# Performance work log

Measured on AMD Instinct MI355X. Metric: run time of the kernel, lower is better.

Reference implementation:

```python
import jax, jax.numpy as jnp
import numpy as np

_S = np.float32(1.0 / np.sqrt(2.0))
_lo = np.array([_S, _S], np.float32)   # dec_lo reversed == rec_lo for db1
_hi = np.array([_S, -_S], np.float32)  # dec_hi reversed == rec_hi for db1
# filters[k][i,j]: k=0 LL/2, k=1 hi(i)*lo(j), k=2 lo(i)*hi(j), k=3 hi*hi  (matches torch unsqueeze outer products)
DEC = np.stack([np.outer(_lo, _lo) / 2.0, np.outer(_hi, _lo), np.outer(_lo, _hi), np.outer(_hi, _hi)]).astype(np.float32)
INV = np.stack([np.outer(_lo, _lo) * 2.0, np.outer(_hi, _lo), np.outer(_lo, _hi), np.outer(_hi, _hi)]).astype(np.float32)
INV_FLIP = np.ascontiguousarray(INV[:, ::-1, ::-1])  # spatially flipped for conv_transpose-as-dilated-conv

DN = ('NCHW', 'OIHW', 'NCHW')


def wt(x):
    # single grouped (depthwise x4) strided conv == per-channel loop in the original
    N, C, H, W = x.shape
    k = jnp.broadcast_to(jnp.asarray(DEC)[None], (C, 4, 2, 2)).reshape(C * 4, 1, 2, 2)
    r = jax.lax.conv_general_dilated(x, k, (2, 2), 'VALID', dimension_numbers=DN, feature_group_count=C)
    r = r.reshape(N, C, 4, H // 2, W // 2)
    r = jnp.concatenate([r[:, :, :1], (r[:, :, 1:] + 1.0) / 2.0], axis=2)  # detail remap
    return r.reshape(N, 4 * C, H // 2, W // 2)


def iwt(v):
    N, C4, H, W = v.shape
    C = C4 // 4
    r = v.reshape(N, C, 4, H, W)
    r = jnp.concatenate([r[:, :, :1], 2.0 * r[:, :, 1:] - 1.0], axis=2).reshape(N, C4, H, W)
    k = jnp.broadcast_to(jnp.asarray(INV_FLIP)[None], (C, 4, 2, 2))
    # conv_transpose2d(stride=2, k=2) == dilated conv with lhs_dilation=2, pad 1, flipped kernel
    return jax.lax.conv_general_dilated(r, k, (1, 1), ((1, 1), (1, 1)), lhs_dilation=(2, 2),
                                        dimension_numbers=DN, feature_group_count=C)


def ws_conv(x, w, b, pad):
    # weight standardization: subtract mean over (in,kh,kw), divide by per-filter std (unbiased) + 1e-5
    wc = w - w.mean(axis=(1, 2, 3), keepdims=True)
    std = wc.reshape(w.shape[0], -1).std(axis=1, ddof=1).reshape(-1, 1, 1, 1) + 1e-5
    y = jax.lax.conv_general_dilated(x, wc / std, (1, 1), ((pad, pad), (pad, pad)), dimension_numbers=DN)
    return y if b is None else y + b[None, :, None, None]


def gn(x, g, b, G):
    N, C, H, W = x.shape
    xr = x.reshape(N, G, -1)
    m = xr.mean(-1, keepdims=True)
    v = xr.var(-1, keepdims=True)
    xr = (xr - m) * jax.lax.rsqrt(v + 1e-5)
    return xr.reshape(N, C, H, W) * g[None, :, None, None] + b[None, :, None, None]


def lrelu(t):
    return jnp.where(t > 0, t, 0.2 * t)


def setup_inputs() -> dict:
    key = jax.random.key(0)
    ks = iter(jax.random.split(key, 32))
    f32 = jnp.float32
    d = {}
    d['x'] = jax.random.normal(next(ks), (16, 3, 256, 256), f32)
    def wgt(shape):
        return 0.05 * jax.random.normal(next(ks), shape, f32)
    def bias(n):
        return 0.01 * jax.random.normal(next(ks), (n,), f32)
    c = 16
    d['conv1_w'], d['conv1_b'] = wgt((c, 12, 3, 3)), bias(c)
    d['conv2_w'], d['conv2_b'] = wgt((4 * c, 4 * c, 3, 3)), bias(4 * c)
    d['conv3_w'], d['conv3_b'] = wgt((16 * c, 16 * c, 3, 3)), bias(16 * c)
    d['conv4_w'], d['conv4_b'] = wgt((64 * c, 64 * c, 3, 3)), bias(64 * c)
    d['convd1_w'], d['convd1_b'] = wgt((12, c, 3, 3)), bias(12)
    d['convd2_w'], d['convd2_b'] = wgt((c, 2 * c, 3, 3)), bias(c)
    d['convd3_w'], d['convd3_b'] = wgt((4 * c, 8 * c, 3, 3)), bias(4 * c)
    d['convd4_w'], d['convd4_b'] = wgt((16 * c, 32 * c, 3, 3)), bias(16 * c)
    d['final_w'] = wgt((2, 3, 1, 1))
    for name, n in (('gn1', c), ('gn2', 4 * c), ('gn3', 16 * c), ('gn4', 64 * c)):
        d[name + '_w'] = 1.0 + 0.1 * jax.random.normal(next(ks), (n,), f32)
        d[name + '_b'] = 0.01 * jax.random.normal(next(ks), (n,), f32)
    return d


def reference(x, conv1_w, conv1_b, conv2_w, conv2_b, conv3_w, conv3_b, conv4_w, conv4_b,
              convd1_w, convd1_b, convd2_w, convd2_b, convd3_w, convd3_b, convd4_w, convd4_b,
              final_w, gn1_w, gn1_b, gn2_w, gn2_b, gn3_w, gn3_b, gn4_w, gn4_b):
    w1 = wt(x)
    c1 = gn(lrelu(ws_conv(w1, conv1_w, conv1_b, 1)), gn1_w, gn1_b, 2)
    w2 = wt(c1)
    c2 = gn(lrelu(ws_conv(w2, conv2_w, conv2_b, 1)), gn2_w, gn2_b, 8)
    w3 = wt(c2)
    c3 = gn(lrelu(ws_conv(w3, conv3_w, conv3_b, 1)), gn3_w, gn3_b, 32)
    w4 = wt(c3)
    c4 = gn(lrelu(ws_conv(w4, conv4_w, conv4_b, 1)), gn4_w, gn4_b, 128)
    c5 = gn(lrelu(ws_conv(c4, conv4_w, conv4_b, 1)), gn4_w, gn4_b, 128)
    c6 = ws_conv(c5, conv4_w, conv4_b, 1)
    ic4 = lrelu(c6 + w4)
    iw4 = jnp.concatenate([c3, iwt(ic4)], axis=1)
    ic3 = gn(lrelu(ws_conv(iw4, convd4_w, convd4_b, 1)), gn3_w, gn3_b, 32)
    iw3 = jnp.concatenate([c2, iwt(ic3)], axis=1)
    ic2 = gn(lrelu(ws_conv(iw3, convd3_w, convd3_b, 1)), gn2_w, gn2_b, 8)
    iw2 = jnp.concatenate([c1, iwt(ic2)], axis=1)
    ic1 = gn(lrelu(ws_conv(iw2, convd2_w, convd2_b, 1)), gn1_w, gn1_b, 2)
    iw1 = lrelu(ws_conv(ic1, convd1_w, convd1_b, 1))
    y = ws_conv(iwt(iw1), final_w, None, 0)
    return y
```

## Files before the change

### kernel.cpp

```cpp
#include <hip/hip_runtime.h>
#include <math.h>


#define NB 16

typedef _Float16 f16;
typedef _Float16 f16x8 __attribute__((ext_vector_type(8)));
typedef _Float16 f16x4 __attribute__((ext_vector_type(4)));
typedef float f32x4 __attribute__((ext_vector_type(4)));
typedef float f32x2 __attribute__((ext_vector_type(2)));
typedef unsigned int u32;

#define LLDS16(gp, lp)                                                          \
  __builtin_amdgcn_global_load_lds((const __attribute__((address_space(1))) u32*)(const void*)(gp), \
                                   (__attribute__((address_space(3))) u32*)(void*)(lp), 16, 0, 0)

__device__ __forceinline__ void ws_reduce(const float* wp, int fan, float* red,
                                          float& mean, float& inv) {
  float s = 0.f, s2 = 0.f;
  for (int i = threadIdx.x; i < fan; i += 256) { float v = wp[i]; s += v; s2 += v * v; }
  red[threadIdx.x] = s; red[256 + threadIdx.x] = s2;
  __syncthreads();
  for (int st = 128; st > 0; st >>= 1) {
    if (threadIdx.x < st) {
      red[threadIdx.x] += red[threadIdx.x + st];
      red[256 + threadIdx.x] += red[256 + threadIdx.x + st];
    }
    __syncthreads();
  }
  float sum = red[0], sumsq = red[256];
  mean = sum / (float)fan;
  float var = (sumsq - sum * mean) / (float)(fan - 1);
  if (var < 0.f) var = 0.f;
  inv = 1.0f / (sqrtf(var) + 1e-5f);
}

__global__ void ws_all_kernel(const float* w0, float* o0, const float* w1, float* o1,
                              const float* w2, float* o2, const float* w3, float* o3) {
  __shared__ float red[512];
  int b = blockIdx.x;
  const float* w; float* o; int fan, oi;
  if (b < 16)      { w = w0; o = o0; fan = 108; oi = b; }
  else if (b < 28) { w = w1; o = o1; fan = 144; oi = b - 16; }
  else if (b < 44) { w = w2; o = o2; fan = 288; oi = b - 28; }
  else             { w = w3; o = o3; fan = 3;   oi = b - 44; }
  const float* wp = w + (size_t)oi * fan;
  float mean, inv; ws_reduce(wp, fan, red, mean, inv);
  for (int i = threadIdx.x; i < fan; i += 256)
    o[(size_t)oi * fan + i] = (wp[i] - mean) * inv;
}

__global__ void ws_f16_all_kernel(const float* w0, f16* o0, const float* w1, f16* o1,
                                  const float* w2, f16* o2, const float* w3, f16* o3,
                                  const float* w4, f16* o4) {
  __shared__ float red[512];
  int b = blockIdx.x;
  const float* w; f16* o; int fan, Cin, Cout, oi;
  if (b < 64)        { w = w0; o = o0; fan = 576;  Cin = 64;   Cout = 64;   oi = b; }
  else if (b < 320)  { w = w1; o = o1; fan = 2304; Cin = 256;  Cout = 256;  oi = b - 64; }
  else if (b < 1344) { w = w2; o = o2; fan = 9216; Cin = 1024; Cout = 1024; oi = b - 320; }
  else if (b < 1408) { w = w3; o = o3; fan = 1152; Cin = 128;  Cout = 64;   oi = b - 1344; }
  else               { w = w4; o = o4; fan = 4608; Cin = 512;  Cout = 256;  oi = b - 1408; }
  const float* wp = w + (size_t)oi * fan;
  float mean, inv; ws_reduce(wp, fan, red, mean, inv);
  for (int i = threadIdx.x; i < fan; i += 256) {
    int ci = i / 9, tap = i - ci * 9;
    o[((size_t)tap * Cout + oi) * Cin + ci] = (f16)((wp[i] - mean) * inv);
  }
}

__device__ __forceinline__ void halo_write(f16* buf, int C, int H, int W, int t) {
  int c8s = C >> 3;
  int c8 = t % c8s; int q = t / c8s;
  int P = 2 * (W + 2) + 2 * H;
  int b = q % P; int n = q / P;
  int y, x;
  if (b < W + 2) { y = 0; x = b; }
  else if (b < 2 * (W + 2)) { y = H + 1; x = b - (W + 2); }
  else { int bb = b - 2 * (W + 2); y = 1 + (bb >> 1); x = (bb & 1) ? (W + 1) : 0; }
  size_t a = (((size_t)n * (H + 2) + y) * (W + 2) + x) * C + c8 * 8;
  *(f16x8*)(buf + a) = (f16x8){0, 0, 0, 0, 0, 0, 0, 0};
}

__global__ void halo2_kernel(f16* b0, int c0, int h0, int w0, int n0,
                             f16* b1, int c1, int h1, int w1, int total) {
  int idx = blockIdx.x * 256 + threadIdx.x;
  if (idx >= total) return;
  if (idx < n0) halo_write(b0, c0, h0, w0, idx);
  else halo_write(b1, c1, h1, w1, idx - n0);
}

__global__ void zero_halo_kernel(f16* __restrict__ buf, int C, int H, int W, int total8) {
  int idx = blockIdx.x * 256 + threadIdx.x;
  if (idx >= total8) return;
  halo_write(buf, C, H, W, idx);
}

__global__ void wt_kernel(const float* __restrict__ in, float* __restrict__ out,
                          int C, int Ho, int Wo, int total) {
  int idx = blockIdx.x * 256 + threadIdx.x;
  if (idx >= total) return;
  int w = idx % Wo; int t = idx / Wo;
  int h = t % Ho; t /= Ho;
  int c = t % C; int n = t / C;
  int Wi = 2 * Wo;
  const float* ip = in + (((size_t)n * C + c) * (2 * Ho) + 2 * h) * Wi + 2 * w;
  float a = ip[0], b = ip[1], cc = ip[Wi], d = ip[Wi + 1];
  size_t cs = (size_t)Ho * Wo;
  float* op = out + (((size_t)n * 4 * C + 4 * c) * Ho + h) * Wo + w;
  op[0]      = 0.25f * (a + b + cc + d);
  op[cs]     = 0.25f * (a + b - cc - d) + 0.5f;
  op[2 * cs] = 0.25f * (a - b + cc - d) + 0.5f;
  op[3 * cs] = 0.25f * (a - b - cc + d) + 0.5f;
}

__global__ __launch_bounds__(256) void wt_nhwc_gn_kernel(
    const float* __restrict__ in, const float* __restrict__ gnp,
    const float* __restrict__ gamma, const float* __restrict__ beta,
    int G, int Sg, int len,
    f16* __restrict__ out, float* __restrict__ out32, float* __restrict__ gnwb,
    int C, int Ho, int Wo) {
  __shared__ f16 sm[32][264];
  __shared__ float scs[8], shs[8];
  int HWo = Ho * Wo;
  int p0 = blockIdx.x * 256, c0 = blockIdx.y * 8, n = blockIdx.z;
  int t = threadIdx.x;
  if (t < 8) {
    int c = c0 + t;
    int g = c / (C / G);
    const float* pp = gnp + (size_t)((n * G + g) * Sg) * 2;
    float s = 0.f, s2 = 0.f;
    for (int i = 0; i < Sg; ++i) { s += pp[2 * i]; s2 += pp[2 * i + 1]; }
    float mean = s / (float)len;
    float var = s2 / (float)len - mean * mean;
    if (var < 0.f) var = 0.f;
    float inv = rsqrtf(var + 1e-5f);
    float ga = gamma[c];
    scs[t] = inv * ga;
    shs[t] = beta[c] - mean * inv * ga;
  }
  __syncthreads();
  int p = p0 + t; int h = p / Wo; int ww = p - h * Wo;
  int Wi = 2 * Wo;
  int C4 = 4 * C;
#pragma unroll
  for (int r = 0; r < 8; ++r) {
    size_t ioff = (((size_t)n * C + c0 + r) * (2 * Ho) + 2 * h) * Wi + 2 * ww;
    const float* ip = in + ioff;
    f32x2 u0 = *(const f32x2*)ip;
    f32x2 u1 = *(const f32x2*)(ip + Wi);
    float sc = scs[r], sh = shs[r];
    float a = u0.x * sc + sh, b = u0.y * sc + sh;
    float cc = u1.x * sc + sh, d = u1.y * sc + sh;
    if (gnwb) {
      float* wp = gnwb + ioff;
      *(f32x2*)wp = (f32x2){a, b};
      *(f32x2*)(wp + Wi) = (f32x2){cc, d};
    }
    float v0 = 0.25f * (a + b + cc + d);
    float v1 = 0.25f * (a + b - cc - d) + 0.5f;
    float v2 = 0.25f * (a - b + cc - d) + 0.5f;
    float v3 = 0.25f * (a - b - cc + d) + 0.5f;
    sm[4 * r][t]     = (f16)v0;
    sm[4 * r + 1][t] = (f16)v1;
    sm[4 * r + 2][t] = (f16)v2;
    sm[4 * r + 3][t] = (f16)v3;
    if (out32) {
      float* op = out32 + (((size_t)n * C4 + 4 * (c0 + r)) * Ho + h) * Wo + ww;
      size_t cs = (size_t)HWo;
      op[0] = v0; op[cs] = v1; op[2 * cs] = v2; op[3 * cs] = v3;
    }
  }
  __syncthreads();
#pragma unroll
  for (int i = 0; i < 4; ++i) {
    int c = t + i * 256;
    int pl = c >> 2, cio = (c & 3) * 8;
    f16x8 v;
#pragma unroll
    for (int u = 0; u < 8; ++u) v[u] = sm[cio + u][pl];
    int pp = p0 + pl; int y = pp / Wo; int x = pp - y * Wo;
    *(f16x8*)(out + (((size_t)n * (Ho + 2) + y + 1) * (Wo + 2) + x + 1) * C4 + c0 * 4 + cio) = v;
  }
}

__global__ void concat_iwt_kernel(const float* __restrict__ skip, const float* __restrict__ v,
                                  float* __restrict__ out, const float* __restrict__ gnp,
                                  const float* __restrict__ gamma, const float* __restrict__ beta,
                                  int G, int Sg, int len, int C, int Hh, int Wh,
                                  int totalA, int total) {
  int idx = blockIdx.x * 256 + threadIdx.x;
  if (idx >= total) return;
  int W = 2 * Wh, H = 2 * Hh; int HWs = H * W;
  if (idx < totalA) {
    int p = idx % HWs; int t = idx / HWs; int c = t % C; int n = t / C;
    out[((size_t)n * 2 * C + c) * HWs + p] = skip[idx];
    return;
  }
  int i2 = idx - totalA;
  int w = i2 % Wh; int t = i2 / Wh; int h = t % Hh; t /= Hh;
  int c = t % C; int n = t / C;
  size_t cs = (size_t)Hh * Wh;
  const float* vp = v + (((size_t)n * 4 * C + 4 * c) * Hh + h) * Wh + w;
  float v0 = vp[0], v1 = vp[cs], v2 = vp[2 * cs], v3 = vp[3 * cs];
  if (gnp) {
    int cpg = (4 * C) / G;
    int g = (4 * c) / cpg;
    const float* pp = gnp + (size_t)((n * G + g) * Sg) * 2;
    float s = 0.f, s2 = 0.f;
    for (int i = 0; i < Sg; ++i) { s += pp[2 * i]; s2 += pp[2 * i + 1]; }
    float mean = s / (float)len;
    float var = s2 / (float)len - mean * mean;
    if (var < 0.f) var = 0.f;
    float inv = rsqrtf(var + 1e-5f);
    v0 = (v0 - mean) * inv * gamma[4 * c]     + beta[4 * c];
    v1 = (v1 - mean) * inv * gamma[4 * c + 1] + beta[4 * c + 1];
    v2 = (v2 - mean) * inv * gamma[4 * c + 2] + beta[4 * c + 2];
    v3 = (v3 - mean) * inv * gamma[4 * c + 3] + beta[4 * c + 3];
  }
  v1 = 2.f * v1 - 1.f; v2 = 2.f * v2 - 1.f; v3 = 2.f * v3 - 1.f;
  float* op = out + (((size_t)n * 2 * C + C + c) * H + 2 * h) * (size_t)W + 2 * w;
  op[0]     = v0 + 0.5f * ( v1 + v2 + v3);
  op[1]     = v0 + 0.5f * ( v1 - v2 - v3);
  op[W]     = v0 + 0.5f * (-v1 + v2 - v3);
  op[W + 1] = v0 + 0.5f * (-v1 - v2 + v3);
}

__global__ __launch_bounds__(256) void to_nhwc_pad_kernel(const float* __restrict__ in,
                                                          f16* __restrict__ out,
                                                          int C, int H, int W) {
  __shared__ f16 sm[32][264];
  int HW = H * W;
  int p0 = blockIdx.x * 256, c0 = blockIdx.y * 32, n = blockIdx.z;
  int t = threadIdx.x;
  const float* ip = in + ((size_t)n * C + c0) * HW + p0;
#pragma unroll 8
  for (int r = 0; r < 32; ++r) sm[r][t] = (f16)ip[(size_t)r * HW + t];
  __syncthreads();
#pragma unroll
  for (int i = 0; i < 4; ++i) {
    int c = t + i * 256;
    int pl = c >> 2, cio = (c & 3) * 8;
    f16x8 v;
#pragma unroll
    for (int u = 0; u < 8; ++u) v[u] = sm[cio + u][pl];
    int p = p0 + pl; int y = p / W; int x = p - y * W;
    *(f16x8*)(out + (((size_t)n * (H + 2) + y + 1) * (W + 2) + x + 1) * C + c0 + cio) = v;
  }
}

__global__ __launch_bounds__(256) void gn_nhwc_kernel(
    const float* __restrict__ in, const float* __restrict__ gnp,
    const float* __restrict__ gamma, const float* __restrict__ beta,
    f16* __restrict__ out, int C, int H, int W, int G, int Sg, int len) {
  __shared__ f16 sm[32][264];
  int HW = H * W;
  int p0 = blockIdx.x * 256, c0 = blockIdx.y * 32, n = blockIdx.z;
  int t = threadIdx.x;
  int cpg = C / G;
  const float* ip = in + ((size_t)n * C + c0) * HW + p0;
#pragma unroll 8
  for (int r = 0; r < 32; ++r) {
    int c = c0 + r; int g = c / cpg;
    const float* pp = gnp + (size_t)((n * G + g) * Sg) * 2;
    float s = 0.f, s2 = 0.f;
    for (int i = 0; i < Sg; ++i) { s += pp[2 * i]; s2 += pp[2 * i + 1]; }
    float mean = s / (float)len;
    float var = s2 / (float)len - mean * mean;
    if (var < 0.f) var = 0.f;
    float inv = rsqrtf(var + 1e-5f);
    float ga = gamma[c], be = beta[c];
    sm[r][t] = (f16)((ip[(size_t)r * HW + t] - mean) * inv * ga + be);
  }
  __syncthreads();
#pragma unroll
  for (int i = 0; i < 4; ++i) {
    int c = t + i * 256;
    int pl = c >> 2, cio = (c & 3) * 8;
    f16x8 v;
#pragma unroll
    for (int u = 0; u < 8; ++u) v[u] = sm[cio + u][pl];
    int p = p0 + pl; int y = p / W; int x = p - y * W;
    *(f16x8*)(out + (((size_t)n * (H + 2) + y + 1) * (W + 2) + x + 1) * C + c0 + cio) = v;
  }
}

__global__ __launch_bounds__(256) void conv_mfma6_kernel(
    const f16* __restrict__ A, const f16* __restrict__ Wp,
    f16* __restrict__ part, int Cin, int H, int W, int Cout, int HW) {
  constexpr int CH = 128 * 64;
  __shared__ f16 Asm[2 * CH];
  __shared__ f16 Bsm[2 * CH];

  const int tid = threadIdx.x;
  const int w = tid >> 6, lane = tid & 63;
  const int m0 = blockIdx.x * 128;
  const int co0 = blockIdx.y * 128;
  const int Wp2 = W + 2;

  const f16* gA[4]; const f16* gB[4];
  int lOff[4];
#pragma unroll
  for (int e = 0; e < 4; ++e) {
    int c = e * 256 + tid;
    int r = c >> 3, j = c & 7;
    int jx = j ^ (r & 7);
    int m = m0 + r; int n = m / HW; int p = m - n * HW;
    int y = p / W; int x = p - y * W;
    gA[e] = A + (((size_t)n * (H + 2) + y + 1) * Wp2 + (x + 1)) * Cin + jx * 8;
    gB[e] = Wp + (size_t)(co0 + r) * Cin + jx * 8;
    lOff[e] = (e * 256 + w * 64) * 8;
  }

  const int wm = w & 1, wn = w >> 1;
  const int lr = lane & 15, quad = lane >> 4;
  int aoffs[4][2], boffs[4][2];
#pragma unroll
  for (int i = 0; i < 4; ++i)
#pragma unroll
    for (int kk = 0; kk < 2; ++kk) {
      int r = wm * 64 + i * 16 + lr;
      int cidx = kk * 4 + quad;
      aoffs[i][kk] = (r * 8 + (cidx ^ (r & 7))) * 8;
      int rb = wn * 64 + i * 16 + lr;
      boffs[i][kk] = (rb * 8 + (cidx ^ (rb & 7))) * 8;
    }

  f32x4 acc[4][4];
#pragma unroll
  for (int i = 0; i < 4; ++i)
#pragma unroll
    for (int j = 0; j < 4; ++j) acc[i][j] = (f32x4){0.f, 0.f, 0.f, 0.f};

  const int kpt = Cin >> 6;
  const int nit = (9 * kpt) / gridDim.z;
  const int it0 = blockIdx.z * nit;
  const size_t bstride = (size_t)Cout * Cin;

  auto stageAB = [&](int it, int sel) {
    int tap = it / kpt, kk = it - tap * kpt;
    int dy = tap / 3 - 1, dx = tap % 3 - 1;
    long offA = ((long)dy * Wp2 + dx) * Cin + (kk << 6);
    long offB = (long)tap * bstride + (kk << 6);
    f16* ab = Asm + sel * CH;
    f16* bb = Bsm + sel * CH;
#pragma unroll
    for (int e = 0; e < 4; ++e) {
      LLDS16(gA[e] + offA, ab + lOff[e]);
      LLDS16(gB[e] + offB, bb + lOff[e]);
    }
  };

  stageAB(it0, 0);
  int sel = 0;
  for (int ii = 0; ii < nit; ++ii) {
    __syncthreads();
    if (ii + 1 < nit) stageAB(it0 + ii + 1, sel ^ 1);
    const f16* ab = Asm + sel * CH;
    const f16* bb = Bsm + sel * CH;
    f16x8 af[4][2], bf[4][2];
#pragma unroll
    for (int i = 0; i < 4; ++i)
#pragma unroll
      for (int kk = 0; kk < 2; ++kk) {
        af[i][kk] = *(const f16x8*)&ab[aoffs[i][kk]];
        bf[i][kk] = *(const f16x8*)&bb[boffs[i][kk]];
      }
#pragma unroll
    for (int kk = 0; kk < 2; ++kk)
#pragma unroll
      for (int i = 0; i < 4; ++i)
#pragma unroll
        for (int j = 0; j < 4; ++j)
          acc[i][j] = __builtin_amdgcn_mfma_f32_16x16x32_f16(af[i][kk], bf[j][kk], acc[i][j], 0, 0, 0);
    sel ^= 1;
  }

  const size_t pbase = (size_t)blockIdx.z * NB * Cout * HW;
#pragma unroll
  for (int i = 0; i < 4; ++i) {
    int mg = m0 + wm * 64 + i * 16 + quad * 4;
    int n = mg / HW, p = mg - n * HW;
#pragma unroll
    for (int j = 0; j < 4; ++j) {
      int co = co0 + wn * 64 + j * 16 + lr;
      f32x4 v = acc[i][j];
      f16x4 h;
#pragma unroll
      for (int r = 0; r < 4; ++r) h[r] = (f16)v[r];
      *(f16x4*)&part[pbase + ((size_t)n * Cout + co) * HW + p] = h;
    }
  }
}

__global__ __launch_bounds__(256) void reduceS_kernel(
    const f16* __restrict__ part, const float* __restrict__ bias,
    const float* __restrict__ add, float* __restrict__ out,
    int Cout, int HW, int S, int do_lrelu, int total4,
    float* __restrict__ gnp, int G, int Sg) {
  __shared__ float red[512];
  int idx = blockIdx.x * 256 + threadIdx.x;
  if (idx >= total4) return;
  size_t sstride = (size_t)NB * Cout * HW;
  int hw4 = HW >> 2;
  int p4 = idx % hw4; int t = idx / hw4;
  int c = t % Cout;
  size_t eoff = (size_t)t * HW + p4 * 4;
  float b = bias[c];
  f32x4 o = {b, b, b, b};
  for (int s = 0; s < S; ++s) {
    f16x4 a = *(const f16x4*)(part + s * sstride + eoff);
#pragma unroll
    for (int r = 0; r < 4; ++r) o[r] += (float)a[r];
  }
  if (add) {
    f32x4 av = *(const f32x4*)(add + eoff);
#pragma unroll
    for (int r = 0; r < 4; ++r) o[r] += av[r];
  }
  if (do_lrelu)
#pragma unroll
    for (int r = 0; r < 4; ++r) o[r] = o[r] > 0.f ? o[r] : 0.2f * o[r];
  *(f32x4*)(out + eoff) = o;
  if (gnp) {
    float ls = o[0] + o[1] + o[2] + o[3];
    float ls2 = o[0]*o[0] + o[1]*o[1] + o[2]*o[2] + o[3]*o[3];
    red[threadIdx.x] = ls; red[256 + threadIdx.x] = ls2;
    __syncthreads();
    for (int st = 128; st > 0; st >>= 1) {
      if (threadIdx.x < st) {
        red[threadIdx.x] += red[threadIdx.x + st];
        red[256 + threadIdx.x] += red[256 + threadIdx.x + st];
      }
      __syncthreads();
    }
    if (threadIdx.x == 0) {
      int flat0 = blockIdx.x * 1024;
      int chw = Cout * HW;
      int n = flat0 / chw;
      int rem = flat0 - n * chw;
      int L = (Cout / G) * HW;
      int g = rem / L;
      int s = (rem - g * L) >> 10;
      gnp[((n * G + g) * Sg + s) * 2] = red[0];
      gnp[((n * G + g) * Sg + s) * 2 + 1] = red[256];
    }
  }
}

__global__ __launch_bounds__(256) void conv_mfma3_kernel(
    const f16* __restrict__ A, const f16* __restrict__ Wp,
    const float* __restrict__ bias, float* __restrict__ out,
    int Cin, int H, int W, int Cout, int HW, int do_lrelu) {
  constexpr int CHA = 128 * 64;
  constexpr int CHB = 64 * 64;
  __shared__ f16 Asm[2 * CHA];
  __shared__ f16 Bsm[2 * CHB];

  const int tid = threadIdx.x;
  const int w = tid >> 6, lane = tid & 63;
  const int m0 = blockIdx.x * 128;
  const int co0 = blockIdx.y * 64;
  const int Wp2 = W + 2;

  const f16* gA[4];
  int lAoff[4];
#pragma unroll
  for (int e = 0; e < 4; ++e) {
    int c = e * 256 + tid;
    int r = c >> 3, j = c & 7;
    int jx = j ^ (r & 7);
    int m = m0 + r; int n = m / HW; int p = m - n * HW;
    int y = p / W; int x = p - y * W;
    gA[e] = A + (((size_t)n * (H + 2) + y + 1) * Wp2 + (x + 1)) * Cin + jx * 8;
    lAoff[e] = (e * 256 + w * 64) * 8;
  }
  const f16* gB[2];
  int lBoff[2];
#pragma unroll
  for (int e = 0; e < 2; ++e) {
    int c = e * 256 + tid;
    int r = c >> 3, j = c & 7;
    int jx = j ^ (r & 7);
    gB[e] = Wp + (size_t)(co0 + r) * Cin + jx * 8;
    lBoff[e] = (e * 256 + w * 64) * 8;
  }

  const int wm = w & 1, wn = w >> 1;
  const int lr = lane & 15, quad = lane >> 4;
  int aoffs[4][2], boffs[2][2];
#pragma unroll
  for (int i = 0; i < 4; ++i)
#pragma unroll
    for (int kk = 0; kk < 2; ++kk) {
      int r = wm * 64 + i * 16 + lr;
      int cidx = kk * 4 + quad;
      aoffs[i][kk] = (r * 8 + (cidx ^ (r & 7))) * 8;
    }
#pragma unroll
  for (int jn = 0; jn < 2; ++jn)
#pragma unroll
    for (int kk = 0; kk < 2; ++kk) {
      int rb = wn * 32 + jn * 16 + lr;
      int cidx = kk * 4 + quad;
      boffs[jn][kk] = (rb * 8 + (cidx ^ (rb & 7))) * 8;
    }

  f32x4 acc[4][2];
#pragma unroll
  for (int i = 0; i < 4; ++i)
#pragma unroll
    for (int jn = 0; jn < 2; ++jn) acc[i][jn] = (f32x4){0.f, 0.f, 0.f, 0.f};

  const int kpt = Cin >> 6;
  const int nit = 9 * kpt;
  const size_t bstride = (size_t)Cout * Cin;

  auto stageAB = [&](int it, int sel) {
    int tap = it / kpt, kk = it - tap * kpt;
    int dy = tap / 3 - 1, dx = tap % 3 - 1;
    long offA = ((long)dy * Wp2 + dx) * Cin + (kk << 6);
    long offB = (long)tap * bstride + (kk << 6);
    f16* ab = Asm + sel * CHA;
    f16* bb = Bsm + sel * CHB;
#pragma unroll
    for (int e = 0; e < 4; ++e) LLDS16(gA[e] + offA, ab + lAoff[e]);
#pragma unroll
    for (int e = 0; e < 2; ++e) LLDS16(gB[e] + offB, bb + lBoff[e]);
  };

  stageAB(0, 0);
  int sel = 0;
  for (int ii = 0; ii < nit; ++ii) {
    __syncthreads();
    if (ii + 1 < nit) stageAB(ii + 1, sel ^ 1);
    const f16* ab = Asm + sel * CHA;
    const f16* bb = Bsm + sel * CHB;
    f16x8 af[4][2], bf[2][2];
#pragma unroll
    for (int i = 0; i < 4; ++i)
#pragma unroll
      for (int kk = 0; kk < 2; ++kk) af[i][kk] = *(const f16x8*)&ab[aoffs[i][kk]];
#pragma unroll
    for (int jn = 0; jn < 2; ++jn)
#pragma unroll
      for (int kk = 0; kk < 2; ++kk) bf[jn][kk] = *(const f16x8*)&bb[boffs[jn][kk]];
#pragma unroll
    for (int kk = 0; kk < 2; ++kk)
#pragma unroll
      for (int i = 0; i < 4; ++i)
#pragma unroll
        for (int jn = 0; jn < 2; ++jn)
          acc[i][jn] = __builtin_amdgcn_mfma_f32_16x16x32_f16(af[i][kk], bf[jn][kk], acc[i][jn], 0, 0, 0);
    sel ^= 1;
  }

#pragma unroll
  for (int i = 0; i < 4; ++i) {
    int mg = m0 + wm * 64 + i * 16 + quad * 4;
    int n = mg / HW, p = mg - n * HW;
#pragma unroll
    for (int jn = 0; jn < 2; ++jn) {
      int co = co0 + wn * 32 + jn * 16 + lr;
      float b = bias[co];
      f32x4 v = acc[i][jn];
#pragma unroll
      for (int r = 0; r < 4; ++r) {
        float u = v[r] + b;
        v[r] = (do_lrelu && u < 0.f) ? 0.2f * u : u;
      }
      *(f32x4*)&out[((size_t)n * Cout + co) * HW + p] = v;
    }
  }
}

template <int CO, int CIC>
__global__ __launch_bounds__(256) void conv3x3_kernel(
    const float* __restrict__ in, const float* __restrict__ wgt,
    const float* __restrict__ bias, float* __restrict__ out,
    int Cin, int H, int W, int Cout, int do_lrelu, float* __restrict__ gnp) {
  __shared__ float sm[CIC][18][18];
  int tiles_x = W >> 4;
  int bt = blockIdx.x;
  int tx0 = (bt % tiles_x) << 4;
  int ty0 = (bt / tiles_x) << 4;
  int co0 = blockIdx.y * CO;
  int n = blockIdx.z;
  int tid = threadIdx.x;
  int lx = tid & 15, ly = tid >> 4;

  float acc[CO];
#pragma unroll
  for (int i = 0; i < CO; i++) acc[i] = 0.f;

  const float* inb = in + (size_t)n * Cin * H * W;

  for (int ci0 = 0; ci0 < Cin; ci0 += CIC) {
    __syncthreads();
    for (int idx = tid; idx < CIC * 324; idx += 256) {
      int ci = idx / 324;
      int r = idx - ci * 324;
      int gy = r / 18, gx = r - gy * 18;
      int iy = ty0 + gy - 1, ix = tx0 + gx - 1;
      float v = 0.f;
      if ((unsigned)iy < (unsigned)H && (unsigned)ix < (unsigned)W)
        v = inb[((size_t)(ci0 + ci)) * H * W + (size_t)iy * W + ix];
      sm[ci][gy][gx] = v;
    }
    __syncthreads();
#pragma unroll
    for (int ci = 0; ci < CIC; ci++) {
      float x00 = sm[ci][ly][lx],     x01 = sm[ci][ly][lx + 1],     x02 = sm[ci][ly][lx + 2];
      float x10 = sm[ci][ly + 1][lx], x11 = sm[ci][ly + 1][lx + 1], x12 = sm[ci][ly + 1][lx + 2];
      float x20 = sm[ci][ly + 2][lx], x21 = sm[ci][ly + 2][lx + 1], x22 = sm[ci][ly + 2][lx + 2];
      const float* wp = wgt + ((size_t)co0 * Cin + (ci0 + ci)) * 9;
#pragma unroll
      for (int co = 0; co < CO; co++) {
        const float* wc = wp + (size_t)co * Cin * 9;
        float a = acc[co];
        a = fmaf(wc[0], x00, a); a = fmaf(wc[1], x01, a); a = fmaf(wc[2], x02, a);
        a = fmaf(wc[3], x10, a); a = fmaf(wc[4], x11, a); a = fmaf(wc[5], x12, a);
        a = fmaf(wc[6], x20, a); a = fmaf(wc[7], x21, a); a = fmaf(wc[8], x22, a);
        acc[co] = a;
      }
    }
  }

  float vout[CO];
#pragma unroll
  for (int co = 0; co < CO; co++) {
    float v = acc[co] + bias[co0 + co];
    if (do_lrelu) v = v > 0.f ? v : 0.2f * v;
    vout[co] = v;
  }

  if (gnp) {
    float p0 = 0.f, q0 = 0.f, p1 = 0.f, q1 = 0.f;
#pragma unroll
    for (int co = 0; co < 8; ++co) { p0 += vout[co]; q0 += vout[co] * vout[co]; }
#pragma unroll
    for (int co = 8; co < CO; ++co) { p1 += vout[co]; q1 += vout[co] * vout[co]; }
    float* red = &sm[0][0][0];
    __syncthreads();
    red[tid] = p0; red[256 + tid] = q0; red[512 + tid] = p1; red[768 + tid] = q1;
    __syncthreads();
    for (int st = 128; st > 0; st >>= 1) {
      if (tid < st) {
        red[tid] += red[tid + st]; red[256 + tid] += red[256 + tid + st];
        red[512 + tid] += red[512 + tid + st]; red[768 + tid] += red[768 + tid + st];
      }
      __syncthreads();
    }
    if (tid == 0) {
      int S = gridDim.x;
      gnp[((n * 2 + 0) * S + blockIdx.x) * 2]     = red[0];
      gnp[((n * 2 + 0) * S + blockIdx.x) * 2 + 1] = red[256];
      gnp[((n * 2 + 1) * S + blockIdx.x) * 2]     = red[512];
      gnp[((n * 2 + 1) * S + blockIdx.x) * 2 + 1] = red[768];
    }
  }

  int oy = ty0 + ly, ox = tx0 + lx;
#pragma unroll
  for (int co = 0; co < CO; co++)
    out[(((size_t)n * Cout + co0 + co) * H + oy) * W + ox] = vout[co];
}

template <int CO, int CIC>
__global__ __launch_bounds__(256) void conv3x3_iwt_kernel(
    const float* __restrict__ in, const float* __restrict__ wgt,
    const float* __restrict__ bias, const float* __restrict__ fw,
    const float* __restrict__ gnp, const float* __restrict__ gamma,
    const float* __restrict__ beta, int G, int Sg, int len,
    float* __restrict__ out, int Cin, int H, int W) {
  __shared__ float sm[CIC][18][18];
  __shared__ float csc[16], csh[16];
  int tiles_x = W >> 4;
  int bt = blockIdx.x;
  int tx0 = (bt % tiles_x) << 4;
  int ty0 = (bt / tiles_x) << 4;
  int n = blockIdx.z;
  int tid = threadIdx.x;
  int lx = tid & 15, ly = tid >> 4;

  if (tid < Cin) {
    int g = tid / (Cin / G);
    const float* pp = gnp + (size_t)((n * G + g) * Sg) * 2;
    float s = 0.f, s2 = 0.f;
    for (int i = 0; i < Sg; ++i) { s += pp[2 * i]; s2 += pp[2 * i + 1]; }
    float mean = s / (float)len;
    float var = s2 / (float)len - mean * mean;
    if (var < 0.f) var = 0.f;
    float inv = rsqrtf(var + 1e-5f);
    float ga = gamma[tid];
    csc[tid] = inv * ga;
    csh[tid] = beta[tid] - mean * inv * ga;
  }
  __syncthreads();

  float acc[CO];
#pragma unroll
  for (int i = 0; i < CO; i++) acc[i] = 0.f;

  const float* inb = in + (size_t)n * Cin * H * W;

  for (int ci0 = 0; ci0 < Cin; ci0 += CIC) {
    __syncthreads();
    for (int idx = tid; idx < CIC * 324; idx += 256) {
      int ci = idx / 324;
      int r = idx - ci * 324;
      int gy = r / 18, gx = r - gy * 18;
      int iy = ty0 + gy - 1, ix = tx0 + gx - 1;
      float v = 0.f;
      if ((unsigned)iy < (unsigned)H && (unsigned)ix < (unsigned)W)
        v = inb[((size_t)(ci0 + ci)) * H * W + (size_t)iy * W + ix] * csc[ci0 + ci] + csh[ci0 + ci];
      sm[ci][gy][gx] = v;
    }
    __syncthreads();
#pragma unroll
    for (int ci = 0; ci < CIC; ci++) {
      float x00 = sm[ci][ly][lx],     x01 = sm[ci][ly][lx + 1],     x02 = sm[ci][ly][lx + 2];
      float x10 = sm[ci][ly + 1][lx], x11 = sm[ci][ly + 1][lx + 1], x12 = sm[ci][ly + 1][lx + 2];
      float x20 = sm[ci][ly + 2][lx], x21 = sm[ci][ly + 2][lx + 1], x22 = sm[ci][ly + 2][lx + 2];
      const float* wp = wgt + (size_t)(ci0 + ci) * 9;
#pragma unroll
      for (int co = 0; co < CO; co++) {
        const float* wc = wp + (size_t)co * Cin * 9;
        float a = acc[co];
        a = fmaf(wc[0], x00, a); a = fmaf(wc[1], x01, a); a = fmaf(wc[2], x02, a);
        a = fmaf(wc[3], x10, a); a = fmaf(wc[4], x11, a); a = fmaf(wc[5], x12, a);
        a = fmaf(wc[6], x20, a); a = fmaf(wc[7], x21, a); a = fmaf(wc[8], x22, a);
        acc[co] = a;
      }
    }
  }

  float vout[CO];
#pragma unroll
  for (int co = 0; co < CO; co++) {
    float v = acc[co] + bias[co];
    vout[co] = v > 0.f ? v : 0.2f * v;
  }

  float y0[3], y1[3], y2[3], y3[3];
#pragma unroll
  for (int c = 0; c < 3; ++c) {
    float v0 = vout[4 * c];
    float v1 = 2.f * vout[4 * c + 1] - 1.f;
    float v2 = 2.f * vout[4 * c + 2] - 1.f;
    float v3 = 2.f * vout[4 * c + 3] - 1.f;
    y0[c] = v0 + 0.5f * ( v1 + v2 + v3);
    y1[c] = v0 + 0.5f * ( v1 - v2 - v3);
    y2[c] = v0 + 0.5f * (-v1 + v2 - v3);
    y3[c] = v0 + 0.5f * (-v1 - v2 + v3);
  }
  float w0 = fw[0], w1 = fw[1], w2 = fw[2], w3 = fw[3], w4 = fw[4], w5 = fw[5];
  int oy = ty0 + ly, ox = tx0 + lx;
  int OW = 2 * W;
  size_t ocs = (size_t)(2 * H) * OW;
  float* o0 = out + (size_t)n * 2 * ocs + (size_t)(2 * oy) * OW + 2 * ox;
  o0[0]      = w0 * y0[0] + w1 * y0[1] + w2 * y0[2];
  o0[1]      = w0 * y1[0] + w1 * y1[1] + w2 * y1[2];
  o0[OW]     = w0 * y2[0] + w1 * y2[1] + w2 * y2[2];
  o0[OW + 1] = w0 * y3[0] + w1 * y3[1] + w2 * y3[2];
  float* o1 = o0 + ocs;
  o1[0]      = w3 * y0[0] + w4 * y0[1] + w5 * y0[2];
  o1[1]      = w3 * y1[0] + w4 * y1[1] + w5 * y1[2];
  o1[OW]     = w3 * y2[0] + w4 * y2[1] + w5 * y2[2];
  o1[OW + 1] = w3 * y3[0] + w4 * y3[1] + w5 * y3[2];
}

__global__ __launch_bounds__(256) void gn_stats_kernel(const float* __restrict__ x,
                                                       float* __restrict__ part,
                                                       int C, int HW, int G, int SPLIT) {
  __shared__ float red[512];
  int gs = blockIdx.x;
  int g = gs / SPLIT, s = gs - g * SPLIT;
  int n = blockIdx.y;
  int cpg = C / G;
  int len = cpg * HW;
  int chunk = len / SPLIT;
  size_t base = ((size_t)n * C + (size_t)g * cpg) * HW + (size_t)s * chunk;
  const f32x4* xp = (const f32x4*)(x + base);
  int chunk4 = chunk >> 2;
  float sm = 0.f, s2 = 0.f;
  for (int i = threadIdx.x; i < chunk4; i += 256) {
    f32x4 v = xp[i];
    sm += v.x + v.y + v.z + v.w;
    s2 += v.x * v.x + v.y * v.y + v.z * v.z + v.w * v.w;
  }
  red[threadIdx.x] = sm; red[256 + threadIdx.x] = s2;
  __syncthreads();
  for (int st = 128; st > 0; st >>= 1) {
    if (threadIdx.x < st) {
      red[threadIdx.x] += red[threadIdx.x + st];
      red[256 + threadIdx.x] += red[256 + threadIdx.x + st];
    }
    __syncthreads();
  }
  if (threadIdx.x == 0) {
    int o = ((n * G + g) * SPLIT + s) * 2;
    part[o] = red[0]; part[o + 1] = red[256];
  }
}


extern "C" void kernel_launch(void* const* d_in, const int* in_sizes, int n_in,
                              void* d_out, int out_size, void* d_ws, size_t ws_size,
                              hipStream_t stream) {
  const float* x        = (const float*)d_in[0];
  const float* conv1_w  = (const float*)d_in[1];
  const float* conv1_b  = (const float*)d_in[2];
  const float* conv2_w  = (const float*)d_in[3];
  const float* conv2_b  = (const float*)d_in[4];
  const float* conv3_w  = (const float*)d_in[5];
  const float* conv3_b  = (const float*)d_in[6];
  const float* conv4_w  = (const float*)d_in[7];
  const float* conv4_b  = (const float*)d_in[8];
  const float* convd1_w = (const float*)d_in[9];
  const float* convd1_b = (const float*)d_in[10];
  const float* convd2_w = (const float*)d_in[11];
  const float* convd2_b = (const float*)d_in[12];
  const float* convd3_w = (const float*)d_in[13];
  const float* convd3_b = (const float*)d_in[14];
  const float* convd4_w = (const float*)d_in[15];
  const float* convd4_b = (const float*)d_in[16];
  const float* final_w  = (const float*)d_in[17];
  const float* gn1_w = (const float*)d_in[18];
  const float* gn1_b = (const float*)d_in[19];
  const float* gn2_w = (const float*)d_in[20];
  const float* gn2_b = (const float*)d_in[21];
  const float* gn3_w = (const float*)d_in[22];
  const float* gn3_b = (const float*)d_in[23];
  const float* gn4_w = (const float*)d_in[24];
  const float* gn4_b = (const float*)d_in[25];

  char* base = (char*)d_ws;
  size_t off = 0;
  auto allocB = [&](size_t bytes) { size_t o = off; off = (off + bytes + 255) & ~(size_t)255; return o; };

  size_t o_sw1  = allocB(16 * 108 * 4);
  size_t o_swd1 = allocB(12 * 144 * 4);
  size_t o_swd2 = allocB(16 * 288 * 4);
  size_t o_swf  = allocB(6 * 4);
  size_t o_pw2  = allocB((size_t)9 * 64 * 64 * 2);
  size_t o_pw3  = allocB((size_t)9 * 256 * 256 * 2);
  size_t o_pw4  = allocB((size_t)9 * 1024 * 1024 * 2);
  size_t o_pwd3 = allocB((size_t)9 * 64 * 128 * 2);
  size_t o_pwd4 = allocB((size_t)9 * 256 * 512 * 2);
  size_t o_R1   = allocB((size_t)NB * 66 * 66 * 128 * 2);
  size_t o_R2   = allocB((size_t)NB * 34 * 34 * 512 * 2);
  size_t o_gnp  = allocB(16384 * 4);
  size_t o_c1 = allocB((size_t)NB * 16 * 128 * 128 * 4);
  size_t o_c2 = allocB((size_t)NB * 64 * 64 * 64 * 4);
  size_t o_c3 = allocB((size_t)NB * 256 * 32 * 32 * 4);
  size_t o_w4 = allocB((size_t)NB * 1024 * 16 * 16 * 4);
  size_t o_t1 = allocB((size_t)NB * 1024 * 16 * 16 * 4);
  size_t o_t2 = allocB((size_t)NB * 512 * 32 * 32 * 4);

  if (off > ws_size) return;

  float* c1 = (float*)(base + o_c1);
  float* c2 = (float*)(base + o_c2);
  float* c3 = (float*)(base + o_c3);
  float* w4 = (float*)(base + o_w4);
  float* t1 = (float*)(base + o_t1);
  float* t2 = (float*)(base + o_t2);
  f16* part  = (f16*)(base + o_R1);
  f16* ah64  = (f16*)(base + o_R1);
  f16* ah128 = (f16*)(base + o_R1);
  f16* ah256 = (f16*)(base + o_R2);
  f16* ah1k  = (f16*)(base + o_R2);
  f16* ah512 = (f16*)(base + o_R2);
  f16* pw2 = (f16*)(base + o_pw2);
  f16* pw3 = (f16*)(base + o_pw3);
  f16* pw4 = (f16*)(base + o_pw4);
  f16* pwd3 = (f16*)(base + o_pwd3);
  f16* pwd4 = (f16*)(base + o_pwd4);
  float* gnp = (float*)(base + o_gnp);

  {
    int n0 = NB * (2 * 66 + 2 * 64) * (64 / 8);
    int n1 = NB * (2 * 34 + 2 * 32) * (256 / 8);
    int tot = n0 + n1;
    halo2_kernel<<<(tot + 255) / 256, 256, 0, stream>>>(ah64, 64, 64, 64, n0,
                                                        ah256, 256, 32, 32, tot);
  }
  ws_all_kernel<<<46, 256, 0, stream>>>(conv1_w, (float*)(base + o_sw1),
                                        convd1_w, (float*)(base + o_swd1),
                                        convd2_w, (float*)(base + o_swd2),
                                        final_w, (float*)(base + o_swf));
  ws_f16_all_kernel<<<1664, 256, 0, stream>>>(conv2_w, pw2, conv3_w, pw3, conv4_w, pw4,
                                              convd3_w, pwd3, convd4_w, pwd4);

  auto prep_nhwc = [&](const float* in, f16* ah, int C, int H, int W, int zero) {
    if (zero) {
      int total8 = NB * (2 * (W + 2) + 2 * H) * (C / 8);
      zero_halo_kernel<<<(total8 + 255) / 256, 256, 0, stream>>>(ah, C, H, W, total8);
    }
    dim3 g((H * W) / 256, C / 32, NB);
    to_nhwc_pad_kernel<<<g, 256, 0, stream>>>(in, ah, C, H, W);
  };
  auto wt_nhwc_gn = [&](const float* in, f16* ah, float* haar32, float* wb,
                        const float* gg, const float* gb, int G, int Sg,
                        int C, int Ho, int Wo) {
    int len = (C / G) * (4 * Ho * Wo);
    dim3 g((Ho * Wo) / 256, C / 8, NB);
    wt_nhwc_gn_kernel<<<g, 256, 0, stream>>>(in, gnp, gg, gb, G, Sg, len,
                                             ah, haar32, wb, C, Ho, Wo);
  };
  auto cm6 = [&](const f16* a, const f16* wt, const float* b, float* dest, const float* add,
                 int Cin, int Hs, int Ws, int Cout, int lr, int G, int Sg) {
    dim3 g((NB * Hs * Ws) / 128, Cout / 128, 2);
    conv_mfma6_kernel<<<g, 256, 0, stream>>>(a, wt, part, Cin, Hs, Ws, Cout, Hs * Ws);
    int total4 = (NB * Cout * Hs * Ws) >> 2;
    reduceS_kernel<<<(total4 + 255) / 256, 256, 0, stream>>>(
        part, b, add, dest, Cout, Hs * Ws, 2, lr, total4, G ? gnp : nullptr, G, Sg);
  };
  auto cm3 = [&](const f16* a, const f16* wt, const float* b, float* o,
                 int Cin, int Hs, int Ws, int Cout, int lr) {
    dim3 g((NB * Hs * Ws) / 128, Cout / 64);
    conv_mfma3_kernel<<<g, 256, 0, stream>>>(a, wt, b, o, Cin, Hs, Ws, Cout, Hs * Ws, lr);
  };
  auto stats = [&](const float* xb, int C, int HW, int G, int SPLIT) {
    dim3 gsd(G * SPLIT, NB);
    gn_stats_kernel<<<gsd, 256, 0, stream>>>(xb, gnp, C, HW, G, SPLIT);
  };
  auto concat_iwt = [&](const float* skip, const float* v, float* out, int C, int Hh, int Wh,
                        const float* gg, const float* gb, int G, int Sg) {
    int totalA = NB * C * 4 * Hh * Wh;
    int total = totalA + NB * C * Hh * Wh;
    int len = G ? ((4 * C) / G) * Hh * Wh : 1;
    concat_iwt_kernel<<<(total + 255) / 256, 256, 0, stream>>>(
        skip, v, out, G ? gnp : nullptr, gg, gb, G, Sg, len, C, Hh, Wh, totalA, total);
  };

  {
    int total = NB * 3 * 128 * 128;
    wt_kernel<<<(total + 255) / 256, 256, 0, stream>>>(x, t1, 3, 128, 128, total);
  }
  {
    dim3 g(64, 1, NB);
    conv3x3_kernel<16, 4><<<g, 256, 0, stream>>>(t1, (float*)(base + o_sw1), conv1_b,
                                                 c1, 12, 128, 128, 16, 1, gnp);
  }
  wt_nhwc_gn(c1, ah64, nullptr, c1, gn1_w, gn1_b, 2, 64, 16, 64, 64);

  cm3(ah64, pw2, conv2_b, c2, 64, 64, 64, 64, 1);
  stats(c2, 64, 4096, 8, 16);
  wt_nhwc_gn(c2, ah256, nullptr, c2, gn2_w, gn2_b, 8, 16, 64, 32, 32);

  cm6(ah256, pw3, conv3_b, c3, nullptr, 256, 32, 32, 256, 1, 32, 8);
  {
    int total8 = NB * (2 * 18 + 2 * 16) * (1024 / 8);
    zero_halo_kernel<<<(total8 + 255) / 256, 256, 0, stream>>>(ah1k, 1024, 16, 16, total8);
  }
  wt_nhwc_gn(c3, ah1k, w4, c3, gn3_w, gn3_b, 32, 8, 256, 16, 16);

  cm6(ah1k, pw4, conv4_b, t1, nullptr, 1024, 16, 16, 1024, 1, 128, 2);
  {
    dim3 g(1, 32, NB);
    gn_nhwc_kernel<<<g, 256, 0, stream>>>(t1, gnp, gn4_w, gn4_b, ah1k, 1024, 16, 16,
                                          128, 2, 2048);
  }
  cm6(ah1k, pw4, conv4_b, t2, nullptr, 1024, 16, 16, 1024, 1, 128, 2);
  {
    dim3 g(1, 32, NB);
    gn_nhwc_kernel<<<g, 256, 0, stream>>>(t2, gnp, gn4_w, gn4_b, ah1k, 1024, 16, 16,
                                          128, 2, 2048);
  }
  cm6(ah1k, pw4, conv4_b, t1, w4, 1024, 16, 16, 1024, 1, 0, 0);

  concat_iwt(c3, t1, t2, 256, 16, 16, nullptr, nullptr, 0, 0);
  prep_nhwc(t2, ah512, 512, 32, 32, 1);
  cm6(ah512, pwd4, convd4_b, t1, nullptr, 512, 32, 32, 256, 1, 32, 8);
  concat_iwt(c2, t1, t2, 64, 32, 32, gn3_w, gn3_b, 32, 8);
  prep_nhwc(t2, ah128, 128, 64, 64, 1);
  cm3(ah128, pwd3, convd3_b, t1, 128, 64, 64, 64, 1);
  stats(t1, 64, 4096, 8, 16);
  concat_iwt(c1, t1, t2, 16, 64, 64, gn2_w, gn2_b, 8, 16);
  {
    dim3 g(64, 1, NB);
    conv3x3_kernel<16, 4><<<g, 256, 0, stream>>>(t2, (float*)(base + o_swd2), convd2_b,
                                                 t1, 32, 128, 128, 16, 1, gnp);
  }
  {
    dim3 g(64, 1, NB);
    conv3x3_iwt_kernel<12, 4><<<g, 256, 0, stream>>>(
        t1, (float*)(base + o_swd1), convd1_b, (float*)(base + o_swf),
        gnp, gn1_w, gn1_b, 2, 64, 8 * 128 * 128, (float*)d_out, 16, 128, 128);
  }
}
```

Baseline: 887.5 us.

## Fuse split-K reduction, concat and inverse Haar into direct NHWC f16 staging

Adds a kernel that builds the padded NHWC f16 conv input straight from the skip tensor and the decoder features. It applies the inverse wavelet, and optionally group-norm affine or the split-K partial-sum reduction with bias, residual add and leaky ReLU, all inside the transpose. This replaces the reduceS, concat_iwt and to_nhwc_pad kernel chain at two decoder levels, removing fp32 intermediate round-trips and launches. The cost is strided, less coalesced gathers of the low-resolution channels, with each output pixel rereading its 4 subband values.

```diff
diff --git a/kernel.cpp b/kernel.cpp
--- a/kernel.cpp
+++ b/kernel.cpp
@@ -226,26 +226,84 @@
   op[W + 1] = v0 + 0.5f * (-v1 - v2 + v3);
 }
 
-__global__ __launch_bounds__(256) void to_nhwc_pad_kernel(const float* __restrict__ in,
-                                                          f16* __restrict__ out,
-                                                          int C, int H, int W) {
+__global__ __launch_bounds__(256) void concat_iwt_nhwc_kernel(
+    const float* __restrict__ skip, const float* __restrict__ v32,
+    const f16* __restrict__ part, const float* __restrict__ bias,
+    const float* __restrict__ add,
+    const float* __restrict__ gnp, const float* __restrict__ gamma,
+    const float* __restrict__ beta, int G, int Sg, int len,
+    f16* __restrict__ out, int C, int Hh, int Wh) {
   __shared__ f16 sm[32][264];
-  int HW = H * W;
-  int p0 = blockIdx.x * 256, c0 = blockIdx.y * 32, n = blockIdx.z;
-  int t = threadIdx.x;
-  const float* ip = in + ((size_t)n * C + c0) * HW + p0;
+  __shared__ float scs[128], shs[128];
+  const int W = 2 * Wh, H = 2 * Hh;
+  const int HWo = H * W, HWh = Hh * Wh;
+  const int C2 = 2 * C;
+  const int p0 = blockIdx.x * 256, c0 = blockIdx.y * 32, n = blockIdx.z;
+  const int t = threadIdx.x;
+  const bool isV = (c0 >= C);
+  if (isV && gnp) {
+    if (t < 128) {
+      int ch = 4 * (c0 - C) + t;
+      int cpg = (4 * C) / G;
+      int g = ch / cpg;
+      const float* pp = gnp + (size_t)((n * G + g) * Sg) * 2;
+      float s = 0.f, s2 = 0.f;
+      for (int i = 0; i < Sg; ++i) { s += pp[2 * i]; s2 += pp[2 * i + 1]; }
+      float mean = s / (float)len;
+      float var = s2 / (float)len - mean * mean;
+      if (var < 0.f) var = 0.f;
+      float inv = rsqrtf(var + 1e-5f);
+      float ga = gamma[ch];
+      scs[t] = inv * ga;
+      shs[t] = beta[ch] - mean * inv * ga;
+    }
+    __syncthreads();
+  }
+  int p = p0 + t; int y = p / W; int x = p - y * W;
+  if (!isV) {
+    const float* sp = skip + ((size_t)n * C + c0) * HWo + p;
 #pragma unroll 8
-  for (int r = 0; r < 32; ++r) sm[r][t] = (f16)ip[(size_t)r * HW + t];
+    for (int r = 0; r < 32; ++r) sm[r][t] = (f16)sp[(size_t)r * HWo];
+  } else {
+    int hh = y >> 1, sy = y & 1, w2 = x >> 1, sx = x & 1;
+    int q = hh * Wh + w2;
+    int Cv = 4 * C;
+    size_t sstr = (size_t)NB * Cv * HWh;
+    int cb4 = 4 * (c0 - C);
+    for (int r = 0; r < 32; ++r) {
+      float vv[4];
+#pragma unroll
+      for (int k = 0; k < 4; ++k) {
+        int cv = cb4 + 4 * r + k;
+        size_t off = ((size_t)n * Cv + cv) * HWh + q;
+        float val;
+        if (part) {
+          val = (float)part[off] + (float)part[sstr + off] + bias[cv];
+          if (add) val += add[off];
+          val = val > 0.f ? val : 0.2f * val;
+        } else {
+          val = v32[off];
+        }
+        if (gnp) val = val * scs[4 * r + k] + shs[4 * r + k];
+        vv[k] = val;
+      }
+      float v1 = 2.f * vv[1] - 1.f, v2 = 2.f * vv[2] - 1.f, v3 = 2.f * vv[3] - 1.f;
+      float a1 = sy ? -v1 : v1;
+      float a2 = sx ? -v2 : v2;
+      float a3 = (sy ^ sx) ? -v3 : v3;
+      sm[r][t] = (f16)(vv[0] + 0.5f * (a1 + a2 + a3));
+    }
+  }
   __syncthreads();
 #pragma unroll
   for (int i = 0; i < 4; ++i) {
     int c = t + i * 256;
     int pl = c >> 2, cio = (c & 3) * 8;
-    f16x8 v;
-#pragma unroll
-    for (int u = 0; u < 8; ++u) v[u] = sm[cio + u][pl];
-    int p = p0 + pl; int y = p / W; int x = p - y * W;
-    *(f16x8*)(out + (((size_t)n * (H + 2) + y + 1) * (W + 2) + x + 1) * C + c0 + cio) = v;
+    f16x8 ov;
+#pragma unroll
+    for (int u = 0; u < 8; ++u) ov[u] = sm[cio + u][pl];
+    int pp = p0 + pl; int yy = pp / W; int xx = pp - yy * W;
+    *(f16x8*)(out + (((size_t)n * (H + 2) + yy + 1) * (W + 2) + xx + 1) * C2 + c0 + cio) = ov;
   }
 }
 
@@ -893,13 +951,9 @@
   ws_f16_all_kernel<<<1664, 256, 0, stream>>>(conv2_w, pw2, conv3_w, pw3, conv4_w, pw4,
                                               convd3_w, pwd3, convd4_w, pwd4);
 
-  auto prep_nhwc = [&](const float* in, f16* ah, int C, int H, int W, int zero) {
-    if (zero) {
-      int total8 = NB * (2 * (W + 2) + 2 * H) * (C / 8);
-      zero_halo_kernel<<<(total8 + 255) / 256, 256, 0, stream>>>(ah, C, H, W, total8);
-    }
-    dim3 g((H * W) / 256, C / 32, NB);
-    to_nhwc_pad_kernel<<<g, 256, 0, stream>>>(in, ah, C, H, W);
+  auto zero_halo = [&](f16* ah, int C, int H, int W) {
+    int total8 = NB * (2 * (W + 2) + 2 * H) * (C / 8);
+    zero_halo_kernel<<<(total8 + 255) / 256, 256, 0, stream>>>(ah, C, H, W, total8);
   };
   auto wt_nhwc_gn = [&](const float* in, f16* ah, float* haar32, float* wb,
                         const float* gg, const float* gb, int G, int Sg,
@@ -909,10 +963,13 @@
     wt_nhwc_gn_kernel<<<g, 256, 0, stream>>>(in, gnp, gg, gb, G, Sg, len,
                                              ah, haar32, wb, C, Ho, Wo);
   };
+  auto cm6conv = [&](const f16* a, const f16* wt, int Cin, int Hs, int Ws, int Cout) {
+    dim3 g((NB * Hs * Ws) / 128, Cout / 128, 2);
+    conv_mfma6_kernel<<<g, 256, 0, stream>>>(a, wt, part, Cin, Hs, Ws, Cout, Hs * Ws);
+  };
   auto cm6 = [&](const f16* a, const f16* wt, const float* b, float* dest, const float* add,
                  int Cin, int Hs, int Ws, int Cout, int lr, int G, int Sg) {
-    dim3 g((NB * Hs * Ws) / 128, Cout / 128, 2);
-    conv_mfma6_kernel<<<g, 256, 0, stream>>>(a, wt, part, Cin, Hs, Ws, Cout, Hs * Ws);
+    cm6conv(a, wt, Cin, Hs, Ws, Cout);
     int total4 = (NB * Cout * Hs * Ws) >> 2;
     reduceS_kernel<<<(total4 + 255) / 256, 256, 0, stream>>>(
         part, b, add, dest, Cout, Hs * Ws, 2, lr, total4, G ? gnp : nullptr, G, Sg);
@@ -926,14 +983,6 @@
     dim3 gsd(G * SPLIT, NB);
     gn_stats_kernel<<<gsd, 256, 0, stream>>>(xb, gnp, C, HW, G, SPLIT);
   };
-  auto concat_iwt = [&](const float* skip, const float* v, float* out, int C, int Hh, int Wh,
-                        const float* gg, const float* gb, int G, int Sg) {
-    int totalA = NB * C * 4 * Hh * Wh;
-    int total = totalA + NB * C * Hh * Wh;
-    int len = G ? ((4 * C) / G) * Hh * Wh : 1;
-    concat_iwt_kernel<<<(total + 255) / 256, 256, 0, stream>>>(
-        skip, v, out, G ? gnp : nullptr, gg, gb, G, Sg, len, C, Hh, Wh, totalA, total);
-  };
 
   {
     int total = NB * 3 * 128 * 128;
@@ -951,10 +1000,7 @@
   wt_nhwc_gn(c2, ah256, nullptr, c2, gn2_w, gn2_b, 8, 16, 64, 32, 32);
 
   cm6(ah256, pw3, conv3_b, c3, nullptr, 256, 32, 32, 256, 1, 32, 8);
-  {
-    int total8 = NB * (2 * 18 + 2 * 16) * (1024 / 8);
-    zero_halo_kernel<<<(total8 + 255) / 256, 256, 0, stream>>>(ah1k, 1024, 16, 16, total8);
-  }
+  zero_halo(ah1k, 1024, 16, 16);
   wt_nhwc_gn(c3, ah1k, w4, c3, gn3_w, gn3_b, 32, 8, 256, 16, 16);
 
   cm6(ah1k, pw4, conv4_b, t1, nullptr, 1024, 16, 16, 1024, 1, 128, 2);
@@ -969,16 +1015,32 @@
     gn_nhwc_kernel<<<g, 256, 0, stream>>>(t2, gnp, gn4_w, gn4_b, ah1k, 1024, 16, 16,
                                           128, 2, 2048);
   }
-  cm6(ah1k, pw4, conv4_b, t1, w4, 1024, 16, 16, 1024, 1, 0, 0);
-
-  concat_iwt(c3, t1, t2, 256, 16, 16, nullptr, nullptr, 0, 0);
-  prep_nhwc(t2, ah512, 512, 32, 32, 1);
+  cm6conv(ah1k, pw4, 1024, 16, 16, 1024);
+
+  zero_halo(ah512, 512, 32, 32);
+  {
+    dim3 g(4, 16, NB);
+    concat_iwt_nhwc_kernel<<<g, 256, 0, stream>>>(
+        c3, nullptr, part, conv4_b, w4,
+        nullptr, nullptr, nullptr, 0, 0, 0, ah512, 256, 16, 16);
+  }
   cm6(ah512, pwd4, convd4_b, t1, nullptr, 512, 32, 32, 256, 1, 32, 8);
-  concat_iwt(c2, t1, t2, 64, 32, 32, gn3_w, gn3_b, 32, 8);
-  prep_nhwc(t2, ah128, 128, 64, 64, 1);
+  zero_halo(ah128, 128, 64, 64);
+  {
+    dim3 g(16, 4, NB);
+    concat_iwt_nhwc_kernel<<<g, 256, 0, stream>>>(
+        c2, t1, nullptr, nullptr, nullptr,
+        gnp, gn3_w, gn3_b, 32, 8, 8192, ah128, 64, 32, 32);
+  }
   cm3(ah128, pwd3, convd3_b, t1, 128, 64, 64, 64, 1);
   stats(t1, 64, 4096, 8, 16);
-  concat_iwt(c1, t1, t2, 16, 64, 64, gn2_w, gn2_b, 8, 16);
+  {
+    int totalA = NB * 16 * 4 * 64 * 64;
+    int total = totalA + NB * 16 * 64 * 64;
+    int len = (64 / 8) * 64 * 64;
+    concat_iwt_kernel<<<(total + 255) / 256, 256, 0, stream>>>(
+        c1, t1, t2, gnp, gn2_w, gn2_b, 8, 16, len, 16, 64, 64, totalA, total);
+  }
   {
     dim3 g(64, 1, NB);
     conv3x3_kernel<16, 4><<<g, 256, 0, stream>>>(t2, (float*)(base + o_swd2), convd2_b,
```

Result: slower. 960.8 us (+8.3%).
